# Optimization experiments

Measured on AMD Instinct MI355X. Metric: run time of the kernel, lower is better.

The kernel has to match this reference:

```python
import jax, jax.numpy as jnp
import numpy as np

EMBED_DIM = 1024
NUM_HEADS = 16
HEAD_DIM = EMBED_DIM // NUM_HEADS
SCALE = HEAD_DIM ** -0.5


def setup_inputs() -> dict:
    key = jax.random.key(0)
    k_x, k_qkv, k_proj = jax.random.split(key, 3)
    x = jax.random.normal(k_x, (2, 2048, EMBED_DIM), dtype=jnp.float32)
    # nn.Linear weights: [out_features, in_features]
    w_qkv = jax.random.normal(k_qkv, (3 * EMBED_DIM, EMBED_DIM), dtype=jnp.float32) * (EMBED_DIM ** -0.5)
    w_proj = jax.random.normal(k_proj, (EMBED_DIM, EMBED_DIM), dtype=jnp.float32) * (EMBED_DIM ** -0.5)
    return {"x": x, "w_qkv": w_qkv, "w_proj": w_proj}


def reference(x, w_qkv, w_proj):
    B, N, C = x.shape
    # fused QKV projection: [B,N,3C]
    qkv = jnp.einsum('bnc,oc->bno', x, w_qkv)
    qkv = qkv.reshape(B, N, 3, NUM_HEADS, HEAD_DIM)
    q, k, v = jnp.moveaxis(qkv, 2, 0)  # each [B, N, H, D]
    q = q.transpose(0, 2, 1, 3)  # [B, H, N, D]
    k = k.transpose(0, 2, 1, 3)
    v = v.transpose(0, 2, 1, 3)
    # scaled dot-product attention (eval mode: dropout_p=0, non-causal)
    scores = jnp.einsum('bhqd,bhkd->bhqk', q, k) * SCALE
    attn = jax.nn.softmax(scores, axis=-1)
    out = jnp.einsum('bhqk,bhkd->bhqd', attn, v)  # [B, H, N, D]
    out = out.transpose(0, 2, 1, 3).reshape(B, N, C)
    return jnp.einsum('bnc,oc->bno', out, w_proj)
```

## Files before the change

kernel.cpp:

```cpp
#include <hip/hip_runtime.h>
#include <hip/hip_bf16.h>

typedef __bf16 bf16;
typedef __bf16 bf16x8 __attribute__((ext_vector_type(8)));
typedef __bf16 bf16x4 __attribute__((ext_vector_type(4)));
typedef _Float16 f16;
typedef _Float16 f16x4 __attribute__((ext_vector_type(4)));
typedef float f32x4 __attribute__((ext_vector_type(4)));

#define MFMA16(a, b, c)    __builtin_amdgcn_mfma_f32_16x16x32_bf16(a, b, c, 0, 0, 0)
#define MFMA16F16(a, b, c) __builtin_amdgcn_mfma_f32_16x16x16f16(a, b, c, 0, 0, 0)

__device__ __forceinline__ void gll(const void* g, void* l) {
    __builtin_amdgcn_global_load_lds(
        (const __attribute__((address_space(1))) unsigned int*)g,
        (__attribute__((address_space(3))) unsigned int*)l, 16, 0, 0);
}

__global__ void cvt_all(const float* __restrict__ x, const float* __restrict__ wq,
                        const float* __restrict__ wp, bf16* __restrict__ xb,
                        bf16* __restrict__ wqb, bf16* __restrict__ wpb) {
    int i = blockIdx.x * 256 + threadIdx.x;
    const float4* s; bf16* d; int j;
    if (i < 1048576)                { s = (const float4*)x;  d = xb;  j = i; }
    else if (i < 1048576 + 786432)  { s = (const float4*)wq; d = wqb; j = i - 1048576; }
    else                            { s = (const float4*)wp; d = wpb; j = i - 1835008; }
    float4 f = s[j];
    bf16x4 o; o[0] = (bf16)f.x; o[1] = (bf16)f.y; o[2] = (bf16)f.z; o[3] = (bf16)f.w;
    ((bf16x4*)d)[j] = o;
}

#define QSCALE 0.18033688f

__global__ __launch_bounds__(256, 3) void gemm_qkv(
    const bf16* __restrict__ A, const bf16* __restrict__ Bm,
    bf16* __restrict__ qo, bf16* __restrict__ ko, f16* __restrict__ vo)
{
    __shared__ bf16 As[2][128 * 32];
    __shared__ bf16 Bs[2][128 * 32];
    const int tid = threadIdx.x;
    const int wave = tid >> 6, lane = tid & 63;
    const int lrow = lane & 15, quad = lane >> 4;
    const int wm = (wave >> 1) * 64, wn = (wave & 1) * 64;
    const int srow = tid >> 2;
    const int scol = ((tid & 3) ^ (srow & 3)) * 8;
    const int fsw = (quad ^ (lrow & 3)) * 8;

    const bf16* Ap = A + (long)(blockIdx.x * 128 + srow) * 1024 + scol;
    const bf16* Bp = Bm + (long)(blockIdx.y * 128 + srow) * 1024 + scol;

    f32x4 acc[4][4] = {};
    const int gm0 = blockIdx.x * 128 + wm;
    const int go0 = blockIdx.y * 128 + wn;

    gll(Ap, &As[0][tid * 8]);  gll(Ap + 64 * 1024, &As[0][2048 + tid * 8]);
    gll(Bp, &Bs[0][tid * 8]);  gll(Bp + 64 * 1024, &Bs[0][2048 + tid * 8]);

    if (blockIdx.y < 16) {
        for (int i = 0; i < 32; i++) {
            const int cur = i & 1;
            __syncthreads();
            if (i < 31) {
                const int k0 = (i + 1) * 32;
                gll(Ap + k0, &As[cur ^ 1][tid * 8]);
                gll(Ap + 64 * 1024 + k0, &As[cur ^ 1][2048 + tid * 8]);
                gll(Bp + k0, &Bs[cur ^ 1][tid * 8]);
                gll(Bp + 64 * 1024 + k0, &Bs[cur ^ 1][2048 + tid * 8]);
            }
            bf16x8 af[4], bfr[4];
#pragma unroll
            for (int ii = 0; ii < 4; ii++) af[ii] = *(const bf16x8*)&As[cur][(wm + ii * 16 + lrow) * 32 + fsw];
#pragma unroll
            for (int j = 0; j < 4; j++) bfr[j] = *(const bf16x8*)&Bs[cur][(wn + j * 16 + lrow) * 32 + fsw];
#pragma unroll
            for (int ii = 0; ii < 4; ii++)
#pragma unroll
                for (int j = 0; j < 4; j++)
                    acc[ii][j] = MFMA16(bfr[j], af[ii], acc[ii][j]);
        }
        const bool isQ = blockIdx.y < 8;
        bf16* dst = isQ ? qo : ko;
        const float sc = isQ ? QSCALE : 1.0f;
#pragma unroll
        for (int i = 0; i < 4; i++) {
            int gm = gm0 + i * 16 + lrow;
            int b = gm >> 11, n = gm & 2047;
#pragma unroll
            for (int j = 0; j < 4; j++) {
                int ob = go0 + j * 16 + quad * 4;
                int rem = ob & 1023;
                int h = rem >> 6, d0 = rem & 63;
                bf16x4 pk;
#pragma unroll
                for (int r = 0; r < 4; r++) pk[r] = (bf16)(acc[i][j][r] * sc);
                *(bf16x4*)&dst[((long)(b * 16 + h) * 2048 + n) * 64 + d0] = pk;
            }
        }
    } else {
        for (int i = 0; i < 32; i++) {
            const int cur = i & 1;
            __syncthreads();
            if (i < 31) {
                const int k0 = (i + 1) * 32;
                gll(Ap + k0, &As[cur ^ 1][tid * 8]);
                gll(Ap + 64 * 1024 + k0, &As[cur ^ 1][2048 + tid * 8]);
                gll(Bp + k0, &Bs[cur ^ 1][tid * 8]);
                gll(Bp + 64 * 1024 + k0, &Bs[cur ^ 1][2048 + tid * 8]);
            }
            bf16x8 af[4], bfr[4];
#pragma unroll
            for (int ii = 0; ii < 4; ii++) af[ii] = *(const bf16x8*)&As[cur][(wm + ii * 16 + lrow) * 32 + fsw];
#pragma unroll
            for (int j = 0; j < 4; j++) bfr[j] = *(const bf16x8*)&Bs[cur][(wn + j * 16 + lrow) * 32 + fsw];
#pragma unroll
            for (int ii = 0; ii < 4; ii++)
#pragma unroll
                for (int j = 0; j < 4; j++)
                    acc[ii][j] = MFMA16(af[ii], bfr[j], acc[ii][j]);
        }
#pragma unroll
        for (int i = 0; i < 4; i++) {
            int gmb = gm0 + i * 16 + quad * 4;
            int b = gmb >> 11, nb = gmb & 2047;
#pragma unroll
            for (int j = 0; j < 4; j++) {
                int o = go0 + j * 16 + lrow;
                int rem = o & 1023;
                int h = rem >> 6, d = rem & 63;
                f16x4 pk;
#pragma unroll
                for (int r = 0; r < 4; r++) pk[r] = (f16)acc[i][j][r];
                *(f16x4*)&vo[(((long)(b * 16 + h)) * 64 + d) * 2048 + nb] = pk;
            }
        }
    }
}

__global__ __launch_bounds__(256, 2) void attn_kernel(
    const bf16* __restrict__ q, const bf16* __restrict__ k,
    const f16* __restrict__ vt, bf16* __restrict__ o)
{
    __shared__ bf16 Ks[2][128 * 64];
    __shared__ f16  Vs[2][64 * 128];

    const int tid = threadIdx.x, wave = tid >> 6, lane = tid & 63;
    const int lrow = lane & 15, quad = lane >> 4;
    const int bh = blockIdx.x & 31, qt = blockIdx.x >> 5;
    const bf16* Qp = q + ((long)bh * 2048 + qt * 128 + wave * 32) * 64;
    const bf16* Kp = k + (long)bh * 2048 * 64;
    const f16*  Vp = vt + (long)bh * 64 * 2048;

    const int srK = tid >> 3, scK = ((tid & 7) ^ (srK & 7)) * 8;
    const int srV = tid >> 4, scV = ((tid & 15) ^ (srV & 15)) * 8;

    bf16x8 qf[2][2];
#pragma unroll
    for (int t = 0; t < 2; t++)
#pragma unroll
        for (int ks = 0; ks < 2; ks++)
            qf[t][ks] = *(const bf16x8*)&Qp[(t * 16 + lrow) * 64 + ks * 32 + quad * 8];

#pragma unroll
    for (int p = 0; p < 4; p++) {
        gll(Kp + (srK + 32 * p) * 64 + scK,          &Ks[0][p * 2048 + tid * 8]);
        gll(Vp + (long)(srV + 16 * p) * 2048 + scV,  &Vs[0][p * 2048 + tid * 8]);
    }

    float lsum[2] = {0.0f, 0.0f};
    f32x4 oacc[2][4] = {};

    for (int kv = 0; kv < 16; kv++) {
        const int cur = kv & 1;
        __syncthreads();
        if (kv < 15) {
            const bf16* Kn = Kp + (kv + 1) * 8192;
            const f16*  Vn = Vp + (kv + 1) * 128;
#pragma unroll
            for (int p = 0; p < 4; p++) {
                gll(Kn + (srK + 32 * p) * 64 + scK,         &Ks[cur ^ 1][p * 2048 + tid * 8]);
                gll(Vn + (long)(srV + 16 * p) * 2048 + scV, &Vs[cur ^ 1][p * 2048 + tid * 8]);
            }
        }

#pragma unroll
        for (int s = 0; s < 2; s++) {
            f32x4 sacc[2][4];
#pragma unroll
            for (int t = 0; t < 2; t++)
#pragma unroll
                for (int n = 0; n < 4; n++) sacc[t][n] = f32x4{-8.f, -8.f, -8.f, -8.f};
#pragma unroll
            for (int ks = 0; ks < 2; ks++) {
                bf16x8 kf[4];
#pragma unroll
                for (int n = 0; n < 4; n++) {
                    int row = s * 64 + n * 16 + lrow;
                    kf[n] = *(const bf16x8*)&Ks[cur][row * 64 + (((ks * 4 + quad) ^ (lrow & 7)) * 8)];
                }
#pragma unroll
                for (int t = 0; t < 2; t++)
#pragma unroll
                    for (int n = 0; n < 4; n++)
                        sacc[t][n] = MFMA16(kf[n], qf[t][ks], sacc[t][n]);
            }

            f16x4 pa[2][4];
#pragma unroll
            for (int t = 0; t < 2; t++)
#pragma unroll
                for (int n = 0; n < 4; n++)
#pragma unroll
                    for (int r = 0; r < 4; r++) {
                        float p = __builtin_exp2f(sacc[t][n][r]);
                        lsum[t] += p;
                        pa[t][n][r] = (f16)p;
                    }

#pragma unroll
            for (int jd = 0; jd < 4; jd++) {
                f16x4 vf[4];
#pragma unroll
                for (int n = 0; n < 4; n++) {
                    int c = s * 8 + n * 2 + (quad >> 1);
                    vf[n] = *(const f16x4*)&Vs[cur][(jd * 16 + lrow) * 128 + (c ^ lrow) * 8 + (quad & 1) * 4];
                }
#pragma unroll
                for (int t = 0; t < 2; t++)
#pragma unroll
                    for (int n = 0; n < 4; n++)
                        oacc[t][jd] = MFMA16F16(pa[t][n], vf[n], oacc[t][jd]);
            }
        }
    }

#pragma unroll
    for (int t = 0; t < 2; t++) {
        lsum[t] += __shfl_xor(lsum[t], 16, 64);
        lsum[t] += __shfl_xor(lsum[t], 32, 64);
    }

    __syncthreads();
    bf16* Pw = ((bf16*)Ks) + wave * 32 * 72;
    const int b = bh >> 4, h = bh & 15;
#pragma unroll
    for (int t = 0; t < 2; t++) {
        float linv = 1.0f / lsum[t];
#pragma unroll
        for (int r = 0; r < 4; r++) {
            float lr = __shfl(linv, quad * 4 + r, 64);
#pragma unroll
            for (int jd = 0; jd < 4; jd++)
                Pw[(t * 16 + quad * 4 + r) * 72 + jd * 16 + lrow] = (bf16)(oacc[t][jd][r] * lr);
        }
    }
    const int rr = lane >> 3, cc = (lane & 7) * 8;
#pragma unroll
    for (int p = 0; p < 4; p++) {
        bf16x8 val = *(const bf16x8*)&Pw[(rr + p * 8) * 72 + cc];
        int n = qt * 128 + wave * 32 + rr + p * 8;
        *(bf16x8*)&o[((long)(b * 2048 + n)) * 1024 + h * 64 + cc] = val;
    }
}

__global__ __launch_bounds__(256, 2) void gemm_proj(
    const bf16* __restrict__ A, const bf16* __restrict__ Bm, float* __restrict__ out)
{
    __shared__ bf16 As[2][128 * 32];
    __shared__ bf16 Bs[2][64 * 32];
    const int tid = threadIdx.x;
    const int wave = tid >> 6, lane = tid & 63;
    const int lrow = lane & 15, quad = lane >> 4;
    const int wm = (wave >> 1) * 64, wn = (wave & 1) * 32;
    const int srow = tid >> 2;
    const int scol = ((tid & 3) ^ (srow & 3)) * 8;
    const int fsw = (quad ^ (lrow & 3)) * 8;

    const bf16* Ap = A + (long)(blockIdx.x * 128 + srow) * 1024 + scol;
    const bf16* Bp = Bm + (long)(blockIdx.y * 64 + srow) * 1024 + scol;

    f32x4 acc[4][2] = {};

    gll(Ap, &As[0][tid * 8]);  gll(Ap + 64 * 1024, &As[0][2048 + tid * 8]);
    gll(Bp, &Bs[0][tid * 8]);

    for (int i = 0; i < 32; i++) {
        const int cur = i & 1;
        __syncthreads();
        if (i < 31) {
            const int k0 = (i + 1) * 32;
            gll(Ap + k0, &As[cur ^ 1][tid * 8]);
            gll(Ap + 64 * 1024 + k0, &As[cur ^ 1][2048 + tid * 8]);
            gll(Bp + k0, &Bs[cur ^ 1][tid * 8]);
        }
        bf16x8 af[4], bfr[2];
#pragma unroll
        for (int ii = 0; ii < 4; ii++) af[ii] = *(const bf16x8*)&As[cur][(wm + ii * 16 + lrow) * 32 + fsw];
#pragma unroll
        for (int j = 0; j < 2; j++) bfr[j] = *(const bf16x8*)&Bs[cur][(wn + j * 16 + lrow) * 32 + fsw];
#pragma unroll
        for (int ii = 0; ii < 4; ii++)
#pragma unroll
            for (int j = 0; j < 2; j++)
                acc[ii][j] = MFMA16(bfr[j], af[ii], acc[ii][j]);
    }

    const int gm0 = blockIdx.x * 128 + wm;
    const int go0 = blockIdx.y * 64 + wn;
#pragma unroll
    for (int i = 0; i < 4; i++) {
        int gm = gm0 + i * 16 + lrow;
#pragma unroll
        for (int j = 0; j < 2; j++) {
            int ob = go0 + j * 16 + quad * 4;
            *(f32x4*)&out[(long)gm * 1024 + ob] = acc[i][j];
        }
    }
}

extern "C" void kernel_launch(void* const* d_in, const int* in_sizes, int n_in,
                              void* d_out, int out_size, void* d_ws, size_t ws_size,
                              hipStream_t stream) {
    const float* x      = (const float*)d_in[0];
    const float* w_qkv  = (const float*)d_in[1];
    const float* w_proj = (const float*)d_in[2];
    float* out = (float*)d_out;

    bf16* ws = (bf16*)d_ws;
    bf16* xb     = ws;
    bf16* wqkvb  = xb + 4096 * 1024;
    bf16* wprojb = wqkvb + 3072 * 1024;
    bf16* qb     = wprojb + 1024 * 1024;
    bf16* kb     = qb + 2 * 16 * 2048 * 64;
    f16*  vb     = (f16*)(kb + 2 * 16 * 2048 * 64);
    bf16* ob     = (bf16*)(vb + 2 * 16 * 2048 * 64);

    cvt_all<<<8192, 256, 0, stream>>>(x, w_qkv, w_proj, xb, wqkvb, wprojb);
    gemm_qkv<<<dim3(32, 24), 256, 0, stream>>>(xb, wqkvb, qb, kb, vb);
    attn_kernel<<<512, 256, 0, stream>>>(qb, kb, vb, ob);
    gemm_proj<<<dim3(32, 16), 256, 0, stream>>>(ob, wprojb, out);
}
```

Measured before the change: 196.3 us.

## Split attention KV range across wave pairs with 64-row Q tiles and LDS reduction

Reorganizes the attention kernel so that each wave owns 64 query rows, and two waves split each 64-key KV tile between them. The KV tile shrinks from 128 to 64 and the loop runs twice as many iterations. Partial output accumulators and row sums are merged through a new LDS buffer at the end before normalization and store. The aim is to halve K/V fragment LDS reads per MFMA by reusing each fragment across more query tiles. The cost is more LDS per block, twice as many barriers, and a final cross-wave reduction.

```diff
diff --git a/kernel.cpp b/kernel.cpp
--- a/kernel.cpp
+++ b/kernel.cpp
@@ -140,125 +140,146 @@
     const bf16* __restrict__ q, const bf16* __restrict__ k,
     const f16* __restrict__ vt, bf16* __restrict__ o)
 {
-    __shared__ bf16 Ks[2][128 * 64];
-    __shared__ f16  Vs[2][64 * 128];
+    __shared__ bf16  Ks[2][64 * 64];
+    __shared__ f16   Vs[2][64 * 64];
+    __shared__ float Pt[2][64 * 68];
+    __shared__ float lsumL[2][64];
 
     const int tid = threadIdx.x, wave = tid >> 6, lane = tid & 63;
     const int lrow = lane & 15, quad = lane >> 4;
+    const int qh = wave & 1, kh = wave >> 1;
     const int bh = blockIdx.x & 31, qt = blockIdx.x >> 5;
-    const bf16* Qp = q + ((long)bh * 2048 + qt * 128 + wave * 32) * 64;
+    const bf16* Qp = q + ((long)bh * 2048 + qt * 128 + qh * 64) * 64;
     const bf16* Kp = k + (long)bh * 2048 * 64;
     const f16*  Vp = vt + (long)bh * 64 * 2048;
 
-    const int srK = tid >> 3, scK = ((tid & 7) ^ (srK & 7)) * 8;
-    const int srV = tid >> 4, scV = ((tid & 15) ^ (srV & 15)) * 8;
-
-    bf16x8 qf[2][2];
-#pragma unroll
-    for (int t = 0; t < 2; t++)
+    const int sr = tid >> 3;
+    const int scc = ((tid & 7) ^ (sr & 7)) * 8;
+
+    bf16x8 qf[4][2];
+#pragma unroll
+    for (int t = 0; t < 4; t++)
 #pragma unroll
         for (int ks = 0; ks < 2; ks++)
             qf[t][ks] = *(const bf16x8*)&Qp[(t * 16 + lrow) * 64 + ks * 32 + quad * 8];
 
 #pragma unroll
-    for (int p = 0; p < 4; p++) {
-        gll(Kp + (srK + 32 * p) * 64 + scK,          &Ks[0][p * 2048 + tid * 8]);
-        gll(Vp + (long)(srV + 16 * p) * 2048 + scV,  &Vs[0][p * 2048 + tid * 8]);
-    }
-
-    float lsum[2] = {0.0f, 0.0f};
-    f32x4 oacc[2][4] = {};
-
-    for (int kv = 0; kv < 16; kv++) {
+    for (int p = 0; p < 2; p++) {
+        gll(Kp + (sr + 32 * p) * 64 + scc,         &Ks[0][p * 2048 + tid * 8]);
+        gll(Vp + (long)(sr + 32 * p) * 2048 + scc, &Vs[0][p * 2048 + tid * 8]);
+    }
+
+    float lsum[4] = {0.f, 0.f, 0.f, 0.f};
+    f32x4 oacc[4][4] = {};
+
+    for (int kv = 0; kv < 32; kv++) {
         const int cur = kv & 1;
         __syncthreads();
-        if (kv < 15) {
-            const bf16* Kn = Kp + (kv + 1) * 8192;
-            const f16*  Vn = Vp + (kv + 1) * 128;
-#pragma unroll
-            for (int p = 0; p < 4; p++) {
-                gll(Kn + (srK + 32 * p) * 64 + scK,         &Ks[cur ^ 1][p * 2048 + tid * 8]);
-                gll(Vn + (long)(srV + 16 * p) * 2048 + scV, &Vs[cur ^ 1][p * 2048 + tid * 8]);
-            }
-        }
-
-#pragma unroll
-        for (int s = 0; s < 2; s++) {
-            f32x4 sacc[2][4];
-#pragma unroll
-            for (int t = 0; t < 2; t++)
-#pragma unroll
-                for (int n = 0; n < 4; n++) sacc[t][n] = f32x4{-8.f, -8.f, -8.f, -8.f};
-#pragma unroll
-            for (int ks = 0; ks < 2; ks++) {
-                bf16x8 kf[4];
-#pragma unroll
-                for (int n = 0; n < 4; n++) {
-                    int row = s * 64 + n * 16 + lrow;
-                    kf[n] = *(const bf16x8*)&Ks[cur][row * 64 + (((ks * 4 + quad) ^ (lrow & 7)) * 8)];
+        if (kv < 31) {
+            const bf16* Kn = Kp + (kv + 1) * 4096;
+            const f16*  Vn = Vp + (kv + 1) * 64;
+#pragma unroll
+            for (int p = 0; p < 2; p++) {
+                gll(Kn + (sr + 32 * p) * 64 + scc,         &Ks[cur ^ 1][p * 2048 + tid * 8]);
+                gll(Vn + (long)(sr + 32 * p) * 2048 + scc, &Vs[cur ^ 1][p * 2048 + tid * 8]);
+            }
+        }
+
+        f32x4 sacc[4][2];
+#pragma unroll
+        for (int t = 0; t < 4; t++)
+#pragma unroll
+            for (int n = 0; n < 2; n++) sacc[t][n] = f32x4{-8.f, -8.f, -8.f, -8.f};
+#pragma unroll
+        for (int ks = 0; ks < 2; ks++) {
+            bf16x8 kf[2];
+#pragma unroll
+            for (int n = 0; n < 2; n++)
+                kf[n] = *(const bf16x8*)&Ks[cur][(kh * 32 + n * 16 + lrow) * 64 +
+                                                 (((ks * 4 + quad) ^ (lrow & 7)) * 8)];
+#pragma unroll
+            for (int t = 0; t < 4; t++)
+#pragma unroll
+                for (int n = 0; n < 2; n++)
+                    sacc[t][n] = MFMA16(kf[n], qf[t][ks], sacc[t][n]);
+        }
+
+        f16x4 pa[4][2];
+#pragma unroll
+        for (int t = 0; t < 4; t++)
+#pragma unroll
+            for (int n = 0; n < 2; n++)
+#pragma unroll
+                for (int r = 0; r < 4; r++) {
+                    float p = __builtin_exp2f(sacc[t][n][r]);
+                    lsum[t] += p;
+                    pa[t][n][r] = (f16)p;
                 }
-#pragma unroll
-                for (int t = 0; t < 2; t++)
-#pragma unroll
-                    for (int n = 0; n < 4; n++)
-                        sacc[t][n] = MFMA16(kf[n], qf[t][ks], sacc[t][n]);
-            }
-
-            f16x4 pa[2][4];
-#pragma unroll
-            for (int t = 0; t < 2; t++)
-#pragma unroll
-                for (int n = 0; n < 4; n++)
-#pragma unroll
-                    for (int r = 0; r < 4; r++) {
-                        float p = __builtin_exp2f(sacc[t][n][r]);
-                        lsum[t] += p;
-                        pa[t][n][r] = (f16)p;
-                    }
-
-#pragma unroll
-            for (int jd = 0; jd < 4; jd++) {
-                f16x4 vf[4];
-#pragma unroll
-                for (int n = 0; n < 4; n++) {
-                    int c = s * 8 + n * 2 + (quad >> 1);
-                    vf[n] = *(const f16x4*)&Vs[cur][(jd * 16 + lrow) * 128 + (c ^ lrow) * 8 + (quad & 1) * 4];
-                }
-#pragma unroll
-                for (int t = 0; t < 2; t++)
-#pragma unroll
-                    for (int n = 0; n < 4; n++)
-                        oacc[t][jd] = MFMA16F16(pa[t][n], vf[n], oacc[t][jd]);
-            }
-        }
-    }
-
-#pragma unroll
-    for (int t = 0; t < 2; t++) {
+
+#pragma unroll
+        for (int jd = 0; jd < 4; jd++) {
+            f16x4 vf[2];
+#pragma unroll
+            for (int n = 0; n < 2; n++) {
+                int cs = kh * 4 + n * 2 + (quad >> 1);
+                vf[n] = *(const f16x4*)&Vs[cur][(jd * 16 + lrow) * 64 +
+                                               ((cs ^ (lrow & 7)) * 8) + (quad & 1) * 4];
+            }
+#pragma unroll
+            for (int t = 0; t < 4; t++)
+#pragma unroll
+                for (int n = 0; n < 2; n++)
+                    oacc[t][jd] = MFMA16F16(pa[t][n], vf[n], oacc[t][jd]);
+        }
+    }
+
+#pragma unroll
+    for (int t = 0; t < 4; t++) {
         lsum[t] += __shfl_xor(lsum[t], 16, 64);
         lsum[t] += __shfl_xor(lsum[t], 32, 64);
     }
 
+    float* Pr = &Pt[qh][0];
+    if (kh == 1) {
+#pragma unroll
+        for (int t = 0; t < 4; t++)
+#pragma unroll
+            for (int jd = 0; jd < 4; jd++)
+                *(f32x4*)&Pr[lane * 68 + (t * 4 + jd) * 4] = oacc[t][jd];
+        if (quad == 0)
+#pragma unroll
+            for (int t = 0; t < 4; t++) lsumL[qh][t * 16 + lrow] = lsum[t];
+    }
     __syncthreads();
-    bf16* Pw = ((bf16*)Ks) + wave * 32 * 72;
-    const int b = bh >> 4, h = bh & 15;
-#pragma unroll
-    for (int t = 0; t < 2; t++) {
-        float linv = 1.0f / lsum[t];
-#pragma unroll
-        for (int r = 0; r < 4; r++) {
-            float lr = __shfl(linv, quad * 4 + r, 64);
+    if (kh == 0) {
+#pragma unroll
+        for (int t = 0; t < 4; t++)
 #pragma unroll
             for (int jd = 0; jd < 4; jd++)
-                Pw[(t * 16 + quad * 4 + r) * 72 + jd * 16 + lrow] = (bf16)(oacc[t][jd][r] * lr);
-        }
-    }
-    const int rr = lane >> 3, cc = (lane & 7) * 8;
-#pragma unroll
-    for (int p = 0; p < 4; p++) {
-        bf16x8 val = *(const bf16x8*)&Pw[(rr + p * 8) * 72 + cc];
-        int n = qt * 128 + wave * 32 + rr + p * 8;
-        *(bf16x8*)&o[((long)(b * 2048 + n)) * 1024 + h * 64 + cc] = val;
+                oacc[t][jd] += *(const f32x4*)&Pr[lane * 68 + (t * 4 + jd) * 4];
+#pragma unroll
+        for (int t = 0; t < 4; t++) lsum[t] += lsumL[qh][t * 16 + lrow];
+
+        bf16* Tw = (bf16*)Pr;
+        const int b = bh >> 4, h = bh & 15;
+#pragma unroll
+        for (int t = 0; t < 4; t++) {
+            float linv = 1.0f / lsum[t];
+#pragma unroll
+            for (int r = 0; r < 4; r++) {
+                float lr = __shfl(linv, quad * 4 + r, 64);
+#pragma unroll
+                for (int jd = 0; jd < 4; jd++)
+                    Tw[(t * 16 + quad * 4 + r) * 72 + jd * 16 + lrow] = (bf16)(oacc[t][jd][r] * lr);
+            }
+        }
+        const int rr = lane >> 3, cc = (lane & 7) * 8;
+#pragma unroll
+        for (int p = 0; p < 8; p++) {
+            bf16x8 val = *(const bf16x8*)&Tw[(rr + p * 8) * 72 + cc];
+            int n = qt * 128 + qh * 64 + rr + p * 8;
+            *(bf16x8*)&o[((long)(b * 2048 + n)) * 1024 + h * 64 + cc] = val;
+        }
     }
 }
 
```

After: 193.3 us. About the same (-1.5%).
